# Performance work log

Measured on AMD Instinct MI355X. Metric: run time of the kernel, lower is better.

Reference implementation:

```python
import jax, jax.numpy as jnp
import numpy as np

N = 10000      # num_nodes (also input feature width per GCNConv(num_nodes, 200))
E = 320000     # num edges (avg degree 32)
H1 = 200
C = 8
N_TEST = 2000


def _gcn_norm(edge_index, edge_weight, num_nodes):
    """PyG GCNConv symmetric normalization with self-loops (fill value 1)."""
    loop = jnp.arange(num_nodes)
    row = jnp.concatenate([edge_index[0], loop])          # source nodes
    col = jnp.concatenate([edge_index[1], loop])          # target nodes
    w = jnp.concatenate([edge_weight, jnp.ones((num_nodes,), edge_weight.dtype)])
    deg = jax.ops.segment_sum(w, col, num_segments=num_nodes)
    dis = jnp.where(deg > 0, jax.lax.rsqrt(deg), 0.0)     # deg^{-1/2}, 0 for isolated
    norm = dis[row] * w * dis[col]
    return row, col, norm


def _gcn_conv(x, row, col, norm, W, b, num_nodes):
    h = x @ W                                             # linear transform first (PyG order)
    msg = h[row] * norm[:, None]                          # gather + scale
    out = jax.ops.segment_sum(msg, col, num_segments=num_nodes)  # scatter-add aggregate
    return out + b


def setup_inputs() -> dict:
    key = jax.random.key(0)
    ks = jax.random.split(key, 8)
    x = jax.random.normal(ks[0], (N, N), jnp.float32)
    edge_index = jax.random.randint(ks[1], (2, E), 0, N, dtype=jnp.int64) if jax.config.read('jax_enable_x64') else jax.random.randint(ks[1], (2, E), 0, N)
    edge_weight = jax.random.uniform(ks[2], (E,), jnp.float32)
    mask_idx = jax.random.randint(ks[3], (N_TEST,), 0, N)
    y = jax.random.randint(ks[4], (N,), 0, C)
    W1 = jax.random.normal(ks[5], (N, H1), jnp.float32) / np.sqrt(N).astype(np.float32)
    b1 = jnp.zeros((H1,), jnp.float32)
    W2 = jax.random.normal(ks[6], (H1, C), jnp.float32) / np.sqrt(H1).astype(np.float32)
    b2 = jnp.zeros((C,), jnp.float32)
    return {"x": x, "edge_index": edge_index, "edge_weight": edge_weight,
            "mask_idx": mask_idx, "y": y, "W1": W1, "b1": b1, "W2": W2, "b2": b2}


def reference(x, edge_index, edge_weight, mask_idx, y, W1, b1, W2, b2):
    row, col, norm = _gcn_norm(edge_index, edge_weight, N)
    h = _gcn_conv(x, row, col, norm, W1, b1, N)
    h = jax.nn.relu(h)
    # dropout: module run in eval mode -> identity
    h = _gcn_conv(h, row, col, norm, W2, b2, N)
    predictions = h[mask_idx]   # masked gather (mode='test')
    targets = y[mask_idx]
    return predictions, targets
```

## Files before the change

### kernel.cpp

```cpp
#include <hip/hip_runtime.h>
#include <hip/hip_bf16.h>

#define NN     10000
#define NE     320000
#define H1DIM  200
#define H1BST  208
#define NCLS   8
#define NTST   2000
#define KDIM   10000
#define KPAD   10048
#define KSPL   6
#define KSTEPS 26
#define NGEMMB 474
#define DPAD   128

typedef __bf16 bf16x8 __attribute__((ext_vector_type(8)));
typedef float  f32x4  __attribute__((ext_vector_type(4)));

__device__ __forceinline__ void load_lds16(const void* g, void* l) {
  __builtin_amdgcn_global_load_lds(
      (__attribute__((address_space(1))) void*)(void*)g,
      (__attribute__((address_space(3))) void*)l, 16, 0, 0);
}


__global__ void k_prep0(float* deg, int* cnt, int* flags,
                        const unsigned* ei, const unsigned* mk, const unsigned* yy,
                        const float* __restrict__ W1, __bf16* __restrict__ Wt) {
  __shared__ float tile[64][65];
  __shared__ int s_f[4];
  int b = blockIdx.x, t = threadIdx.x;
  if (b < 40) {
    int i = b * 256 + t;
    if (i < NN) { deg[i] = 1.0f; cnt[i] = 0; }
    return;
  }
  if (b < 43) {
    unsigned a = 0;
    if (b == 40)      { for (int i = t; i < 2048; i += 256) a |= ei[2 * i + 1]; }
    else if (b == 41) { for (int i = t; i < 2048; i += 256) a |= yy[2 * i + 1]; }
    else              { for (int i = t; i < 900;  i += 256) a |= mk[2 * i + 1]; }
    int wid = t >> 6;
    int any = __any(a != 0) ? 1 : 0;
    if ((t & 63) == 0) s_f[wid] = any;
    __syncthreads();
    if (t == 0) {
      int f = s_f[0] | s_f[1] | s_f[2] | s_f[3];
      int idx = (b == 40) ? 0 : (b == 41) ? 2 : 1;
      flags[idx] = f;
    }
    return;
  }
  int bt = b - 43;
  int k0 = (bt % 157) * 64, n0 = (bt / 157) * 64;
  int tn = t & 63, tk = t >> 6;
  for (int r = 0; r < 64; r += 4) {
    int k = k0 + tk + r, n = n0 + tn;
    tile[tk + r][tn] = (k < KDIM && n < H1DIM) ? W1[k * H1DIM + n] : 0.f;
  }
  __syncthreads();
  for (int r = 0; r < 64; r += 4) {
    int n = n0 + tk + r, k = k0 + tn;
    if (k < KPAD && n < 256)
      Wt[(size_t)n * KPAD + k] = (__bf16)tile[tn][tk + r];
  }
}


__launch_bounds__(512, 4)
__global__ void k_gemm_cvt(const float* __restrict__ x, const __bf16* __restrict__ Wt,
                           __bf16* __restrict__ hpart,
                           const void* ei, const void* mk, const void* yy,
                           const float* __restrict__ ew, const int* __restrict__ flags,
                           int* idx32, int* mask32, int* y32, float* deg, int* cnt,
                           int* eids_pad) {
  int t = threadIdx.x;
  if (blockIdx.x >= NGEMMB) {
    int i = (blockIdx.x - NGEMMB) * 512 + t;
    if (i < NE) {
      int v = (flags[0] == 0) ? (int)((const long long*)ei)[i] : ((const int*)ei)[i];
      idx32[i] = min(max(v, 0), NN - 1);
    } else if (i < 2 * NE) {
      int v = (flags[0] == 0) ? (int)((const long long*)ei)[i] : ((const int*)ei)[i];
      v = min(max(v, 0), NN - 1);
      idx32[i] = v;
      atomicAdd(&deg[v], ew[i - NE]);
      int pos = atomicAdd(&cnt[v], 1);
      if (pos < DPAD) eids_pad[v * DPAD + pos] = i - NE;
    } else if (i < 2 * NE + NTST) {
      int j = i - 2 * NE;
      int v = (flags[1] == 0) ? (int)((const long long*)mk)[j] : ((const int*)mk)[j];
      mask32[j] = min(max(v, 0), NN - 1);
    } else if (i < 2 * NE + NTST + NN) {
      int j = i - 2 * NE - NTST;
      int v = (flags[2] == 0) ? (int)((const long long*)yy)[j] : ((const int*)yy)[j];
      y32[j] = min(max(v, 0), NN - 1);
    }
    return;
  }

  __shared__ __align__(16) __bf16 As[128 * 64];
  __shared__ __align__(16) __bf16 Bs[256 * 64];
  int wv = t >> 6, lane = t & 63;
  int wm = wv >> 2, wn = wv & 3;
  int m0 = (blockIdx.x % 79) * 128;
  int split = blockIdx.x / 79;
  int kbeg = split * (KSTEPS * 64);
  int nsteps = KSTEPS + ((split == KSPL - 1) ? 1 : 0);

  f32x4 acc[4][4];
  #pragma unroll
  for (int i = 0; i < 4; ++i)
    #pragma unroll
    for (int j = 0; j < 4; ++j)
      #pragma unroll
      for (int r = 0; r < 4; ++r) acc[i][j][r] = 0.f;

  int am = t >> 2;
  int ac = t & 3;
  long arow = m0 + am; if (arow >= NN) arow = NN - 1;
  const float* aptr = x + (size_t)arow * KDIM + ac * 16;
  int ag0 = (2 * ac + 0) ^ (am & 7);
  int ag1 = (2 * ac + 1) ^ (am & 7);
  __bf16* awr0 = As + am * 64 + ag0 * 8;
  __bf16* awr1 = As + am * 64 + ag1 * 8;

  const __bf16* bsrc[4];
  __bf16* bdst[4];
  #pragma unroll
  for (int pass = 0; pass < 4; ++pass) {
    int s = pass * 512 + t;
    int brow = s >> 3, bg = s & 7;
    bsrc[pass] = Wt + (size_t)brow * KPAD + ((bg ^ (brow & 7)) * 8);
    bdst[pass] = Bs + (size_t)(pass * 512 + wv * 64) * 8;
  }

  int lrow = lane & 15;
  int lhi = lane >> 4;
  int lx7 = lane & 7;

  float4 v0, v1, v2, v3;
  {
    bool pr = (kbeg + ac * 16 + 16 <= KDIM);
    if (pr) {
      const float4* p = (const float4*)(aptr + kbeg);
      v0 = p[0]; v1 = p[1]; v2 = p[2]; v3 = p[3];
    }
  }

  for (int ks = 0; ks < nsteps; ++ks) {
    int k0 = kbeg + ks * 64;
    #pragma unroll
    for (int pass = 0; pass < 4; ++pass)
      load_lds16(bsrc[pass] + k0, bdst[pass]);
    {
      bool pr = (k0 + ac * 16 + 16 <= KDIM);
      bf16x8 bva, bvb;
      if (pr) {
        bva[0] = (__bf16)v0.x; bva[1] = (__bf16)v0.y;
        bva[2] = (__bf16)v0.z; bva[3] = (__bf16)v0.w;
        bva[4] = (__bf16)v1.x; bva[5] = (__bf16)v1.y;
        bva[6] = (__bf16)v1.z; bva[7] = (__bf16)v1.w;
        bvb[0] = (__bf16)v2.x; bvb[1] = (__bf16)v2.y;
        bvb[2] = (__bf16)v2.z; bvb[3] = (__bf16)v2.w;
        bvb[4] = (__bf16)v3.x; bvb[5] = (__bf16)v3.y;
        bvb[6] = (__bf16)v3.z; bvb[7] = (__bf16)v3.w;
      } else {
        #pragma unroll
        for (int q = 0; q < 8; ++q) { bva[q] = (__bf16)0.f; bvb[q] = (__bf16)0.f; }
      }
      *(bf16x8*)awr0 = bva;
      *(bf16x8*)awr1 = bvb;
    }
    __syncthreads();

    if (ks + 1 < nsteps) {
      int k1 = k0 + 64;
      bool pr = (k1 + ac * 16 + 16 <= KDIM);
      if (pr) {
        const float4* p = (const float4*)(aptr + k1);
        v0 = p[0]; v1 = p[1]; v2 = p[2]; v3 = p[3];
      }
    }

    #pragma unroll
    for (int kk = 0; kk < 2; ++kk) {
      int gs8 = ((kk * 4 + lhi) ^ lx7) * 8;
      bf16x8 af[4], bf[4];
      #pragma unroll
      for (int i = 0; i < 4; ++i)
        af[i] = *(const bf16x8*)&As[(wm * 64 + i * 16 + lrow) * 64 + gs8];
      #pragma unroll
      for (int j = 0; j < 4; ++j)
        bf[j] = *(const bf16x8*)&Bs[(wn * 64 + j * 16 + lrow) * 64 + gs8];
      #pragma unroll
      for (int i = 0; i < 4; ++i)
        #pragma unroll
        for (int j = 0; j < 4; ++j)
          acc[i][j] = __builtin_amdgcn_mfma_f32_16x16x32_bf16(af[i], bf[j], acc[i][j], 0, 0, 0);
    }
    __syncthreads();
  }

  __bf16* outp = hpart + (size_t)split * NN * H1BST;
  int colb = wn * 64 + (lane & 15);
  int rbase = m0 + wm * 64 + ((lane >> 4) * 4);
  #pragma unroll
  for (int i = 0; i < 4; ++i)
    #pragma unroll
    for (int j = 0; j < 4; ++j) {
      int cg = colb + j * 16;
      if (cg < H1BST) {
        #pragma unroll
        for (int r = 0; r < 4; ++r) {
          int rg = rbase + i * 16 + r;
          if (rg < NN) outp[(size_t)rg * H1BST + cg] = (__bf16)acc[i][j][r];
        }
      }
    }
}


__global__ void k_dis_red(const float* __restrict__ deg, float* dis,
                          const __bf16* __restrict__ hpart, __bf16* __restrict__ h1b) {
  int t = threadIdx.x;
  if (blockIdx.x == 254) {
    for (int base = 0; base < NN; base += 1024) {
      int idx = base + t;
      if (idx < NN) { float d = deg[idx]; dis[idx] = (d > 0.f) ? rsqrtf(d) : 0.f; }
    }
    return;
  }
  int i = blockIdx.x * 1024 + t;
  if (i < NN * 26) {
    int c = i / 26, ch = i - c * 26;
    size_t base = (size_t)c * H1BST + ch * 8;
    float s[8];
    #pragma unroll
    for (int q = 0; q < 8; ++q) s[q] = 0.f;
    #pragma unroll
    for (int sp = 0; sp < KSPL; ++sp) {
      bf16x8 v = *(const bf16x8*)(hpart + (size_t)sp * NN * H1BST + base);
      #pragma unroll
      for (int q = 0; q < 8; ++q) s[q] += (float)v[q];
    }
    bf16x8 o;
    #pragma unroll
    for (int q = 0; q < 8; ++q) o[q] = (__bf16)s[q];
    *(bf16x8*)&h1b[base] = o;
  }
}


__global__ void k_agg1lin2(const __bf16* __restrict__ h1b, const float* __restrict__ dis,
                           const float* __restrict__ ew, const int* __restrict__ rows,
                           const int* __restrict__ cnt, const int* __restrict__ eids_pad,
                           const float* __restrict__ b1, const float* __restrict__ W2,
                           float* __restrict__ h2) {
  __shared__ int   s_r[DPAD];
  __shared__ float s_n[DPAD];
  __shared__ float s_acc[8][26][8];
  __shared__ float s_p[26][8];
  int c = blockIdx.x;
  int t = threadIdx.x;
  int len = min(cnt[c], DPAD);
  if (t < len) {
    int e = eids_pad[c * DPAD + t];
    int r = rows[e];
    s_r[t] = r;
    s_n[t] = ew[e] * dis[r];
  }
  __syncthreads();

  int es = t >> 5;
  int f8 = t & 31;
  float acc8[8];
  #pragma unroll
  for (int q = 0; q < 8; ++q) acc8[q] = 0.f;
  if (f8 < 26) {
    for (int j = es; j < len; j += 8) {
      float nv = s_n[j];
      bf16x8 v = *(const bf16x8*)&h1b[(size_t)s_r[j] * H1BST + f8 * 8];
      #pragma unroll
      for (int q = 0; q < 8; ++q) acc8[q] += nv * (float)v[q];
    }
    #pragma unroll
    for (int q = 0; q < 8; ++q) s_acc[es][f8][q] = acc8[q];
  }
  __syncthreads();

  if (es == 0 && f8 < 26) {
    bf16x8 selfv = *(const bf16x8*)&h1b[(size_t)c * H1BST + f8 * 8];
    float d = dis[c];
    float dd = d * d;
    float a[8];
    #pragma unroll
    for (int q = 0; q < 8; ++q) {
      float s = 0.f;
      #pragma unroll
      for (int e2 = 0; e2 < 8; ++e2) s += s_acc[e2][f8][q];
      int feat = f8 * 8 + q;
      if (feat < H1DIM) {
        float av = s * d + dd * (float)selfv[q] + b1[feat];
        a[q] = fmaxf(av, 0.f);
      } else {
        a[q] = 0.f;
      }
    }
    float p[8];
    #pragma unroll
    for (int o = 0; o < 8; ++o) p[o] = 0.f;
    #pragma unroll
    for (int q = 0; q < 8; ++q) {
      int feat = f8 * 8 + q;
      if (feat < H1DIM) {
        float4 wa = *(const float4*)&W2[feat * 8];
        float4 wb = *(const float4*)&W2[feat * 8 + 4];
        p[0] += a[q] * wa.x; p[1] += a[q] * wa.y;
        p[2] += a[q] * wa.z; p[3] += a[q] * wa.w;
        p[4] += a[q] * wb.x; p[5] += a[q] * wb.y;
        p[6] += a[q] * wb.z; p[7] += a[q] * wb.w;
      }
    }
    #pragma unroll
    for (int o = 0; o < 8; ++o) s_p[f8][o] = p[o];
  }
  __syncthreads();

  if (t < 8) {
    float s = 0.f;
    #pragma unroll
    for (int q = 0; q < 26; ++q) s += s_p[q][t];
    h2[(size_t)c * 8 + t] = s;
  }
}


__global__ void k_agg2out(const float* __restrict__ h2, const float* __restrict__ dis,
                          const float* __restrict__ ew, const int* __restrict__ rows,
                          const int* __restrict__ cnt, const int* __restrict__ eids_pad,
                          const float* __restrict__ b2, const int* __restrict__ mask,
                          const int* __restrict__ yv, float* __restrict__ out) {
  int i = blockIdx.x * 256 + threadIdx.x;
  if (i < NTST * NCLS) {
    int r = i >> 3, o = i & 7;
    int c = mask[r];
    float d = dis[c];
    float acc = 0.f;
    int len = min(cnt[c], DPAD);
    for (int j = 0; j < len; ++j) {
      int e = eids_pad[c * DPAD + j];
      int rr = rows[e];
      acc += ew[e] * dis[rr] * h2[rr * NCLS + o];
    }
    out[i] = acc * d + d * d * h2[c * NCLS + o] + b2[o];
  } else if (i < NTST * NCLS + NTST) {
    int r = i - NTST * NCLS;
    out[i] = (float)yv[mask[r]];
  }
}


extern "C" void kernel_launch(void* const* d_in, const int* in_sizes, int n_in,
                              void* d_out, int out_size, void* d_ws, size_t ws_size,
                              hipStream_t stream) {
  const float* x    = (const float*)d_in[0];
  const void*  ei   = d_in[1];
  const float* ew   = (const float*)d_in[2];
  const void*  mask = d_in[3];
  const void*  y    = d_in[4];
  const float* W1   = (const float*)d_in[5];
  const float* b1   = (const float*)d_in[6];
  const float* W2   = (const float*)d_in[7];
  const float* b2   = (const float*)d_in[8];
  float* out = (float*)d_out;

  char* ws = (char*)d_ws;
  float* deg    = (float*)(ws + 0);
  float* dis    = (float*)(ws + (64 << 10));
  int*   idx32  = (int*)(ws + (2 << 20));
  float* h2     = (float*)(ws + (5 << 20));
  int*   mask32 = (int*)(ws + (6 << 20));
  int*   y32    = (int*)(ws + (6 << 20) + (64 << 10));
  int*   flags  = (int*)(ws + (6 << 20) + (128 << 10));
  int*   cnt    = (int*)(ws + (6 << 20) + (256 << 10));
  __bf16* Wt    = (__bf16*)(ws + ((size_t)9 << 20));
  __bf16* h1b   = (__bf16*)(ws + ((size_t)16 << 20));
  __bf16* hpart = (__bf16*)(ws + ((size_t)24 << 20));
  int* eids_pad = (int*)(ws + ((size_t)52 << 20));

  int* rows32 = idx32;

  k_prep0<<<dim3(671), dim3(256), 0, stream>>>(deg, cnt, flags,
                                               (const unsigned*)ei, (const unsigned*)mask,
                                               (const unsigned*)y, W1, Wt);

  k_gemm_cvt<<<dim3(NGEMMB + 1274), dim3(512), 0, stream>>>(
      x, Wt, hpart, ei, mask, y, ew, flags, idx32, mask32, y32, deg, cnt, eids_pad);

  k_dis_red<<<dim3(255), dim3(1024), 0, stream>>>(deg, dis, hpart, h1b);

  k_agg1lin2<<<dim3(10000), dim3(256), 0, stream>>>(h1b, dis, ew, rows32, cnt, eids_pad,
                                                    b1, W2, h2);
  k_agg2out<<<dim3(71), dim3(256), 0, stream>>>(h2, dis, ew, rows32, cnt, eids_pad, b2,
                                                mask32, y32, out);
}
```

Measured before the change: 223.4 us.

## Retile GEMM to 64-row M tiles with 128-wide K steps and fewer splits

The x@W1 GEMM block tile changes from 128x256 with a K step of 64 to 64x256 with a K step of 128. B is staged into two LDS halves, the A swizzle is widened to 16 groups, and the K-split count drops from 6 to 3. Each wave now covers all 64 rows and a 32-column slice. The aim is fewer split partials to write and reduce and fewer barriers per unit of K, at the cost of more B reloads per output row because M tiles are smaller. KPAD and the W1 transpose grid grow to cover the longer K range, and k_dis_red may still assume 6 partial splits.

After: 225.0 us. About the same (+0.7%).

```diff
diff --git a/kernel.cpp b/kernel.cpp
--- a/kernel.cpp
+++ b/kernel.cpp
@@ -8,10 +8,10 @@
 #define NCLS   8
 #define NTST   2000
 #define KDIM   10000
-#define KPAD   10048
-#define KSPL   6
+#define KPAD   10112
+#define KSPL   3
 #define KSTEPS 26
-#define NGEMMB 474
+#define NGEMMB 471
 #define DPAD   128
 
 typedef __bf16 bf16x8 __attribute__((ext_vector_type(8)));
@@ -52,7 +52,7 @@
     return;
   }
   int bt = b - 43;
-  int k0 = (bt % 157) * 64, n0 = (bt / 157) * 64;
+  int k0 = (bt % 158) * 64, n0 = (bt / 158) * 64;
   int tn = t & 63, tk = t >> 6;
   for (int r = 0; r < 64; r += 4) {
     int k = k0 + tk + r, n = n0 + tn;
@@ -99,40 +99,40 @@
     return;
   }
 
-  __shared__ __align__(16) __bf16 As[128 * 64];
-  __shared__ __align__(16) __bf16 Bs[256 * 64];
+  __shared__ __align__(16) __bf16 As[64 * 128];
+  __shared__ __align__(16) __bf16 Bs[2][256 * 64];
   int wv = t >> 6, lane = t & 63;
-  int wm = wv >> 2, wn = wv & 3;
-  int m0 = (blockIdx.x % 79) * 128;
-  int split = blockIdx.x / 79;
-  int kbeg = split * (KSTEPS * 64);
+  int wn = wv;
+  int m0 = (blockIdx.x % 157) * 64;
+  int split = blockIdx.x / 157;
+  int kbeg = split * (KSTEPS * 128);
   int nsteps = KSTEPS + ((split == KSPL - 1) ? 1 : 0);
 
-  f32x4 acc[4][4];
+  f32x4 acc[4][2];
   #pragma unroll
   for (int i = 0; i < 4; ++i)
     #pragma unroll
-    for (int j = 0; j < 4; ++j)
+    for (int j = 0; j < 2; ++j)
       #pragma unroll
       for (int r = 0; r < 4; ++r) acc[i][j][r] = 0.f;
 
-  int am = t >> 2;
-  int ac = t & 3;
-  long arow = m0 + am; if (arow >= NN) arow = NN - 1;
-  const float* aptr = x + (size_t)arow * KDIM + ac * 16;
-  int ag0 = (2 * ac + 0) ^ (am & 7);
-  int ag1 = (2 * ac + 1) ^ (am & 7);
-  __bf16* awr0 = As + am * 64 + ag0 * 8;
-  __bf16* awr1 = As + am * 64 + ag1 * 8;
+  int ar = t >> 3;
+  int acx = t & 7;
+  long arow = m0 + ar; if (arow >= NN) arow = NN - 1;
+  const float* aptr = x + (size_t)arow * KDIM + acx * 16;
+  int ag0 = (2 * acx + 0) ^ (ar & 15);
+  int ag1 = (2 * acx + 1) ^ (ar & 15);
+  __bf16* awr0 = As + ar * 128 + ag0 * 8;
+  __bf16* awr1 = As + ar * 128 + ag1 * 8;
 
   const __bf16* bsrc[4];
-  __bf16* bdst[4];
+  int bdoff[4];
   #pragma unroll
   for (int pass = 0; pass < 4; ++pass) {
     int s = pass * 512 + t;
     int brow = s >> 3, bg = s & 7;
     bsrc[pass] = Wt + (size_t)brow * KPAD + ((bg ^ (brow & 7)) * 8);
-    bdst[pass] = Bs + (size_t)(pass * 512 + wv * 64) * 8;
+    bdoff[pass] = (pass * 512 + wv * 64) * 8;
   }
 
   int lrow = lane & 15;
@@ -141,7 +141,7 @@
 
   float4 v0, v1, v2, v3;
   {
-    bool pr = (kbeg + ac * 16 + 16 <= KDIM);
+    bool pr = (kbeg + acx * 16 + 16 <= KDIM);
     if (pr) {
       const float4* p = (const float4*)(aptr + kbeg);
       v0 = p[0]; v1 = p[1]; v2 = p[2]; v3 = p[3];
@@ -149,12 +149,15 @@
   }
 
   for (int ks = 0; ks < nsteps; ++ks) {
-    int k0 = kbeg + ks * 64;
+    int k0 = kbeg + ks * 128;
     #pragma unroll
     for (int pass = 0; pass < 4; ++pass)
-      load_lds16(bsrc[pass] + k0, bdst[pass]);
+      load_lds16(bsrc[pass] + k0, (void*)(&Bs[0][0] + bdoff[pass]));
+    #pragma unroll
+    for (int pass = 0; pass < 4; ++pass)
+      load_lds16(bsrc[pass] + k0 + 64, (void*)(&Bs[1][0] + bdoff[pass]));
     {
-      bool pr = (k0 + ac * 16 + 16 <= KDIM);
+      bool pr = (k0 + acx * 16 + 16 <= KDIM);
       bf16x8 bva, bvb;
       if (pr) {
         bva[0] = (__bf16)v0.x; bva[1] = (__bf16)v0.y;
@@ -175,8 +178,8 @@
     __syncthreads();
 
     if (ks + 1 < nsteps) {
-      int k1 = k0 + 64;
-      bool pr = (k1 + ac * 16 + 16 <= KDIM);
+      int k1 = k0 + 128;
+      bool pr = (k1 + acx * 16 + 16 <= KDIM);
       if (pr) {
         const float4* p = (const float4*)(aptr + k1);
         v0 = p[0]; v1 = p[1]; v2 = p[2]; v3 = p[3];
@@ -184,31 +187,33 @@
     }
 
     #pragma unroll
-    for (int kk = 0; kk < 2; ++kk) {
-      int gs8 = ((kk * 4 + lhi) ^ lx7) * 8;
-      bf16x8 af[4], bf[4];
+    for (int kk = 0; kk < 4; ++kk) {
+      int gA = ((kk * 4 + lhi) ^ lrow) * 8;
+      int gB = (((kk & 1) * 4 + lhi) ^ lx7) * 8;
+      const __bf16* bbase = &Bs[kk >> 1][0];
+      bf16x8 af[4], bf[2];
       #pragma unroll
       for (int i = 0; i < 4; ++i)
-        af[i] = *(const bf16x8*)&As[(wm * 64 + i * 16 + lrow) * 64 + gs8];
-      #pragma unroll
-      for (int j = 0; j < 4; ++j)
-        bf[j] = *(const bf16x8*)&Bs[(wn * 64 + j * 16 + lrow) * 64 + gs8];
+        af[i] = *(const bf16x8*)&As[(i * 16 + lrow) * 128 + gA];
+      #pragma unroll
+      for (int j = 0; j < 2; ++j)
+        bf[j] = *(const bf16x8*)&bbase[(wn * 32 + j * 16 + lrow) * 64 + gB];
       #pragma unroll
       for (int i = 0; i < 4; ++i)
         #pragma unroll
-        for (int j = 0; j < 4; ++j)
+        for (int j = 0; j < 2; ++j)
           acc[i][j] = __builtin_amdgcn_mfma_f32_16x16x32_bf16(af[i], bf[j], acc[i][j], 0, 0, 0);
     }
     __syncthreads();
   }
 
   __bf16* outp = hpart + (size_t)split * NN * H1BST;
-  int colb = wn * 64 + (lane & 15);
-  int rbase = m0 + wm * 64 + ((lane >> 4) * 4);
+  int colb = wn * 32 + (lane & 15);
+  int rbase = m0 + ((lane >> 4) * 4);
   #pragma unroll
   for (int i = 0; i < 4; ++i)
     #pragma unroll
-    for (int j = 0; j < 4; ++j) {
+    for (int j = 0; j < 2; ++j) {
       int cg = colb + j * 16;
       if (cg < H1BST) {
         #pragma unroll
@@ -391,7 +396,7 @@
 
   int* rows32 = idx32;
 
-  k_prep0<<<dim3(671), dim3(256), 0, stream>>>(deg, cnt, flags,
+  k_prep0<<<dim3(675), dim3(256), 0, stream>>>(deg, cnt, flags,
                                                (const unsigned*)ei, (const unsigned*)mask,
                                                (const unsigned*)y, W1, Wt);
 
```
